# Performance work log

Hardware: AMD Instinct MI355X
Metric: run time of the kernel (lower is better)

The kernel has to match this reference:

```python
import jax, jax.numpy as jnp
import numpy as np


def _w2_1d(u, v):
    """Squared W2 distance between two 1D densities on grid positions arange(n)/n."""
    u = u / (jnp.sum(u) + 1e-10)
    v = v / (jnp.sum(v) + 1e-10)
    u_cdf = jnp.cumsum(u)                       # [n]
    v_cdf = jnp.cumsum(v)                       # [n]
    qs = jnp.sort(jnp.concatenate([u_cdf, v_cdf]))  # [2n]
    n = u.shape[0]
    pos = jnp.arange(n, dtype=u.dtype) / n      # support positions (n == m here)
    # quantile functions via searchsorted (side='left', same as torch default) + clamped gather
    u_q = pos[jnp.clip(jnp.searchsorted(u_cdf, qs), 0, n - 1)]
    v_q = pos[jnp.clip(jnp.searchsorted(v_cdf, qs), 0, n - 1)]
    delta = jnp.diff(qs, prepend=0.0)           # qs padded with leading zero, then diff
    return jnp.sum(delta * (u_q - v_q) ** 2)    # p = 2


def setup_inputs() -> dict:
    key = jax.random.key(0)
    k1, k2 = jax.random.split(key)
    B, S, T, R = 4, 8, 2048, 256
    x = jax.random.normal(k1, (B, S, T, R), dtype=jnp.float32)
    y = jax.random.normal(k2, (B, S, T, R), dtype=jnp.float32)
    return {"x": x, "y": y}


def reference(x, y):
    B, S, T, R = x.shape
    # transform_nonnegative, method='linear': shift by 1.1 * global min (if negative)
    mn = jnp.minimum(jnp.min(x), jnp.min(y))
    mn = jnp.where(mn < 0, mn, jnp.zeros((), x.dtype))
    x = x - 1.1 * mn
    y = y - 1.1 * mn
    # normalize along time axis (dim=2), sum-to-1
    x = x / jnp.sum(x, axis=2, keepdims=True)
    y = y / jnp.sum(y, axis=2, keepdims=True)
    # flatten (B, S, R) problems; each 1D distribution lives along the time axis
    xr = jnp.transpose(x, (0, 1, 3, 2)).reshape(-1, T)  # [B*S*R, T]
    yr = jnp.transpose(y, (0, 1, 3, 2)).reshape(-1, T)
    w2 = jax.vmap(_w2_1d)(xr, yr).reshape(B, S, R)
    return jnp.sum(w2, axis=(1, 2))  # loss per batch element, shape [B]
```

## Files before the change

### kernel.cpp

```cpp
#include <hip/hip_runtime.h>

#define T_N 2048
#define R_N 256
#define SLICES 32
#define NELEM (SLICES * T_N * R_N)
#define INFV 3.0e38f
#define MIN_BLOCKS 2048
#define MIN_THREADS (MIN_BLOCKS * 256)
#define LSTR 2056

#define XS(e) ((e) ^ (((e) >> 5) & 31))

__global__ __launch_bounds__(256) void kmin(const float* __restrict__ x,
                                            const float* __restrict__ y,
                                            float* __restrict__ partial,
                                            float* __restrict__ out) {
    if (blockIdx.x == 0 && threadIdx.x < 4) out[threadIdx.x] = 0.0f;
    const int g0 = blockIdx.x * 256 + threadIdx.x;
    const float4* __restrict__ x4 = (const float4*)x;
    const float4* __restrict__ y4 = (const float4*)y;
    float m0 = INFV, m1 = INFV;
    #pragma unroll
    for (int half = 0; half < 2; ++half) {
        float4 va[4], vb[4];
        #pragma unroll
        for (int it = 0; it < 4; ++it) {
            const int idx = g0 + (half * 4 + it) * MIN_THREADS;
            va[it] = x4[idx];
            vb[it] = y4[idx];
        }
        #pragma unroll
        for (int it = 0; it < 4; ++it) {
            m0 = fminf(m0, fminf(fminf(va[it].x, va[it].y), fminf(va[it].z, va[it].w)));
            m1 = fminf(m1, fminf(fminf(vb[it].x, vb[it].y), fminf(vb[it].z, vb[it].w)));
        }
    }
    float m = fminf(m0, m1);
    #pragma unroll
    for (int off = 32; off; off >>= 1) m = fminf(m, __shfl_down(m, off));
    __shared__ float sm[4];
    if ((threadIdx.x & 63) == 0) sm[threadIdx.x >> 6] = m;
    __syncthreads();
    if (threadIdx.x == 0)
        partial[blockIdx.x] = fminf(fminf(sm[0], sm[1]), fminf(sm[2], sm[3]));
}

__global__ __launch_bounds__(1024, 8) void kmain(const float* __restrict__ x,
                                                 const float* __restrict__ y,
                                                 const float* __restrict__ partial,
                                                 float* __restrict__ out) {
    __shared__ float L[8 * LSTR];
    __shared__ float red16[16];
    __shared__ float psum[4][2][4];
    __shared__ float pacc[4][4];

    const int tid = threadIdx.x;
    const int w = tid >> 6;
    const int lane = tid & 63;

    {
        float m = fminf(partial[tid], partial[tid + 1024]);
        #pragma unroll
        for (int off = 32; off; off >>= 1) m = fminf(m, __shfl_down(m, off));
        if (lane == 0) red16[w] = m;
    }
    __syncthreads();
    float mn = red16[0];
    #pragma unroll
    for (int k = 1; k < 16; ++k) mn = fminf(mn, red16[k]);
    const float sh = 1.1f * fminf(mn, 0.0f);

    const int blk = blockIdx.x;
    const int xcd = blk & 7;
    const int k2 = blk >> 3;
    const int sub = k2 & 3;
    const int rest = k2 >> 2;
    const int rt = (((rest & 1) << 3) + xcd) * 4 + sub;
    const int bs = rest >> 1;
    const size_t base = (size_t)bs * (T_N * R_N) + (size_t)(rt * 4);

    if (tid < 64) L[(tid >> 3) * LSTR + T_N + (tid & 7)] = INFV;

    #pragma unroll
    for (int it = 0; it < 2; ++it) {
        const int t = tid + 1024 * it;
        const int ts = XS(t);
        const float4 a = *(const float4*)(x + base + (size_t)t * R_N);
        const float4 b = *(const float4*)(y + base + (size_t)t * R_N);
        L[0 * LSTR + ts] = a.x - sh;  L[2 * LSTR + ts] = a.y - sh;
        L[4 * LSTR + ts] = a.z - sh;  L[6 * LSTR + ts] = a.w - sh;
        L[1 * LSTR + ts] = b.x - sh;  L[3 * LSTR + ts] = b.y - sh;
        L[5 * LSTR + ts] = b.z - sh;  L[7 * LSTR + ts] = b.w - sh;
    }
    __syncthreads();

    const int p  = w >> 2;
    const int wl = w & 3;
    const int pl = (wl << 6) | lane;
    float* __restrict__ cu = &L[(2 * p) * LSTR];
    float* __restrict__ cv = &L[(2 * p + 1) * LSTR];

    {
        int off8[8];
        #pragma unroll
        for (int k = 0; k < 8; ++k) off8[k] = XS(8 * pl + k);
        float uu[8], vv8[8];
        float su = 0.f, sv = 0.f;
        #pragma unroll
        for (int k = 0; k < 8; ++k) { uu[k] = cu[off8[k]]; su += uu[k]; }
        #pragma unroll
        for (int k = 0; k < 8; ++k) { vv8[k] = cv[off8[k]]; sv += vv8[k]; }
        float iu = su, iv = sv;
        #pragma unroll
        for (int off = 1; off < 64; off <<= 1) {
            const float a = __shfl_up(iu, off);
            const float b = __shfl_up(iv, off);
            if (lane >= off) { iu += a; iv += b; }
        }
        if (lane == 63) { psum[p][0][wl] = iu; psum[p][1][wl] = iv; }
        __syncthreads();
        float prefU = 0.f, totU = 0.f, prefV = 0.f, totV = 0.f;
        #pragma unroll
        for (int k = 0; k < 4; ++k) {
            const float a = psum[p][0][k], b = psum[p][1][k];
            totU += a; totV += b;
            if (k < wl) { prefU += a; prefV += b; }
        }
        const float invU = 1.0f / totU, invV = 1.0f / totV;
        float ru = prefU + (iu - su);
        float rv = prefV + (iv - sv);
        #pragma unroll
        for (int k = 0; k < 8; ++k) { ru += uu[k];  cu[off8[k]] = ru * invU; }
        #pragma unroll
        for (int k = 0; k < 8; ++k) { rv += vv8[k]; cv[off8[k]] = rv * invV; }
    }
    __syncthreads();

    const int d = pl << 4;
    int i = 0, j = 0;
    if (d > 0) {
        int lo = (d > T_N) ? (d - T_N) : 0;
        int hi = (d < T_N) ? d : T_N;
        while (lo < hi) {
            const int mid = (lo + hi) >> 1;
            if (cu[XS(mid)] <= cv[XS(d - mid - 1)]) lo = mid + 1; else hi = mid;
        }
        i = lo; j = d - lo;
    }
    float qprev = 0.0f;
    if (d > 0) {
        const float pa_ = (i > 0) ? cu[XS(i - 1)] : -INFV;
        const float pb_ = (j > 0) ? cv[XS(j - 1)] : -INFV;
        qprev = fmaxf(pa_, pb_);
    }

    float uv = cu[XS(i)];
    float vv = cv[XS(j)];
    float acc = 0.0f;
    #pragma unroll
    for (int s = 0; s < 16; ++s) {
        const bool take = (uv <= vv);
        const float q = fminf(uv, vv);
        const float dd = (float)(min(i, T_N - 1) - min(j, T_N - 1));
        acc += (q - qprev) * dd * dd;
        qprev = q;
        i += take ? 1 : 0;
        j += take ? 0 : 1;
        if (s < 15) {
            const int ni = take ? i : j;
            const float* bp = take ? cu : cv;
            const float r = bp[XS(ni)];
            uv = take ? r : uv;
            vv = take ? vv : r;
        }
    }

    #pragma unroll
    for (int off = 32; off; off >>= 1) acc += __shfl_down(acc, off);
    if (lane == 0) pacc[p][wl] = acc;
    __syncthreads();
    if (tid == 0) {
        float r = 0.f;
        #pragma unroll
        for (int pp = 0; pp < 4; ++pp)
            r += (pacc[pp][0] + pacc[pp][1]) + (pacc[pp][2] + pacc[pp][3]);
        atomicAdd(&out[bs >> 3], r * (1.0f / ((float)T_N * (float)T_N)));
    }
}

extern "C" void kernel_launch(void* const* d_in, const int* in_sizes, int n_in,
                              void* d_out, int out_size, void* d_ws, size_t ws_size,
                              hipStream_t stream) {
    const float* x = (const float*)d_in[0];
    const float* y = (const float*)d_in[1];
    float* out = (float*)d_out;
    float* partial = (float*)d_ws;

    kmin<<<MIN_BLOCKS, 256, 0, stream>>>(x, y, partial, out);
    kmain<<<SLICES * 64, 1024, 0, stream>>>(x, y, partial, out);
}
```

Measured before the change: 210.7 us.

## Overlap global loads with min reduction, use DPP and float2 LDS accesses

Issues the four float4 global loads for each thread's two adjacent time rows before the global-min reduction, so load latency overlaps the partial-min reduce and the first barrier. The shuffle-based min reduction is replaced with DPP row operations. The LDS swizzle is changed to keep element pairs adjacent, which allows float2 LDS stores during staging and float2 loads and stores in the cumulative-sum phase. Each thread now handles consecutive rows rather than strided ones, which changes the global coalescing pattern. This also risks bank conflicts under the new swizzle.

```diff
diff --git a/kernel.cpp b/kernel.cpp
--- a/kernel.cpp
+++ b/kernel.cpp
@@ -9,7 +9,11 @@
 #define MIN_THREADS (MIN_BLOCKS * 256)
 #define LSTR 2056
 
-#define XS(e) ((e) ^ (((e) >> 5) & 31))
+#define XS(e) ((e) ^ (((e) >> 4) & 30))
+
+#define DPPMIN(x, ctrl, rmask)                                                 \
+    fminf((x), __int_as_float(__builtin_amdgcn_update_dpp(                     \
+        0x7f800000, __float_as_int(x), (ctrl), (rmask), 0xf, false)))
 
 __global__ __launch_bounds__(256) void kmin(const float* __restrict__ x,
                                             const float* __restrict__ y,
@@ -49,7 +53,7 @@
                                                  const float* __restrict__ y,
                                                  const float* __restrict__ partial,
                                                  float* __restrict__ out) {
-    __shared__ float L[8 * LSTR];
+    __shared__ __align__(16) float L[8 * LSTR];
     __shared__ float red16[16];
     __shared__ float psum[4][2][4];
     __shared__ float pacc[4][4];
@@ -57,18 +61,6 @@
     const int tid = threadIdx.x;
     const int w = tid >> 6;
     const int lane = tid & 63;
-
-    {
-        float m = fminf(partial[tid], partial[tid + 1024]);
-        #pragma unroll
-        for (int off = 32; off; off >>= 1) m = fminf(m, __shfl_down(m, off));
-        if (lane == 0) red16[w] = m;
-    }
-    __syncthreads();
-    float mn = red16[0];
-    #pragma unroll
-    for (int k = 1; k < 16; ++k) mn = fminf(mn, red16[k]);
-    const float sh = 1.1f * fminf(mn, 0.0f);
 
     const int blk = blockIdx.x;
     const int xcd = blk & 7;
@@ -79,18 +71,39 @@
     const int bs = rest >> 1;
     const size_t base = (size_t)bs * (T_N * R_N) + (size_t)(rt * 4);
 
+    const int r0 = tid << 1;
+    const float4 a0 = *(const float4*)(x + base + (size_t)r0 * R_N);
+    const float4 a1 = *(const float4*)(x + base + (size_t)(r0 + 1) * R_N);
+    const float4 b0 = *(const float4*)(y + base + (size_t)r0 * R_N);
+    const float4 b1 = *(const float4*)(y + base + (size_t)(r0 + 1) * R_N);
+
+    {
+        float m = fminf(partial[tid], partial[tid + 1024]);
+        m = DPPMIN(m, 0x111, 0xf);
+        m = DPPMIN(m, 0x112, 0xf);
+        m = DPPMIN(m, 0x114, 0xf);
+        m = DPPMIN(m, 0x118, 0xf);
+        m = DPPMIN(m, 0x142, 0xa);
+        m = DPPMIN(m, 0x143, 0xc);
+        if (lane == 63) red16[w] = m;
+    }
     if (tid < 64) L[(tid >> 3) * LSTR + T_N + (tid & 7)] = INFV;
-
-    #pragma unroll
-    for (int it = 0; it < 2; ++it) {
-        const int t = tid + 1024 * it;
-        const int ts = XS(t);
-        const float4 a = *(const float4*)(x + base + (size_t)t * R_N);
-        const float4 b = *(const float4*)(y + base + (size_t)t * R_N);
-        L[0 * LSTR + ts] = a.x - sh;  L[2 * LSTR + ts] = a.y - sh;
-        L[4 * LSTR + ts] = a.z - sh;  L[6 * LSTR + ts] = a.w - sh;
-        L[1 * LSTR + ts] = b.x - sh;  L[3 * LSTR + ts] = b.y - sh;
-        L[5 * LSTR + ts] = b.z - sh;  L[7 * LSTR + ts] = b.w - sh;
+    __syncthreads();
+    float mn = red16[0];
+    #pragma unroll
+    for (int k = 1; k < 16; ++k) mn = fminf(mn, red16[k]);
+    const float sh = 1.1f * fminf(mn, 0.0f);
+
+    {
+        const int ws_ = XS(r0);
+        *(float2*)&L[0 * LSTR + ws_] = make_float2(a0.x - sh, a1.x - sh);
+        *(float2*)&L[2 * LSTR + ws_] = make_float2(a0.y - sh, a1.y - sh);
+        *(float2*)&L[4 * LSTR + ws_] = make_float2(a0.z - sh, a1.z - sh);
+        *(float2*)&L[6 * LSTR + ws_] = make_float2(a0.w - sh, a1.w - sh);
+        *(float2*)&L[1 * LSTR + ws_] = make_float2(b0.x - sh, b1.x - sh);
+        *(float2*)&L[3 * LSTR + ws_] = make_float2(b0.y - sh, b1.y - sh);
+        *(float2*)&L[5 * LSTR + ws_] = make_float2(b0.z - sh, b1.z - sh);
+        *(float2*)&L[7 * LSTR + ws_] = make_float2(b0.w - sh, b1.w - sh);
     }
     __syncthreads();
 
@@ -101,15 +114,25 @@
     float* __restrict__ cv = &L[(2 * p + 1) * LSTR];
 
     {
-        int off8[8];
-        #pragma unroll
-        for (int k = 0; k < 8; ++k) off8[k] = XS(8 * pl + k);
+        int offp[4];
+        #pragma unroll
+        for (int c = 0; c < 4; ++c) offp[c] = XS(8 * pl + 2 * c);
         float uu[8], vv8[8];
         float su = 0.f, sv = 0.f;
         #pragma unroll
-        for (int k = 0; k < 8; ++k) { uu[k] = cu[off8[k]]; su += uu[k]; }
-        #pragma unroll
-        for (int k = 0; k < 8; ++k) { vv8[k] = cv[off8[k]]; sv += vv8[k]; }
+        for (int c = 0; c < 4; ++c) {
+            const float2 t2 = *(const float2*)&cu[offp[c]];
+            uu[2 * c] = t2.x; uu[2 * c + 1] = t2.y;
+        }
+        #pragma unroll
+        for (int k = 0; k < 8; ++k) su += uu[k];
+        #pragma unroll
+        for (int c = 0; c < 4; ++c) {
+            const float2 t2 = *(const float2*)&cv[offp[c]];
+            vv8[2 * c] = t2.x; vv8[2 * c + 1] = t2.y;
+        }
+        #pragma unroll
+        for (int k = 0; k < 8; ++k) sv += vv8[k];
         float iu = su, iv = sv;
         #pragma unroll
         for (int off = 1; off < 64; off <<= 1) {
@@ -130,9 +153,19 @@
         float ru = prefU + (iu - su);
         float rv = prefV + (iv - sv);
         #pragma unroll
-        for (int k = 0; k < 8; ++k) { ru += uu[k];  cu[off8[k]] = ru * invU; }
-        #pragma unroll
-        for (int k = 0; k < 8; ++k) { rv += vv8[k]; cv[off8[k]] = rv * invV; }
+        for (int c = 0; c < 4; ++c) {
+            const float ra = ru + uu[2 * c];
+            const float rb = ra + uu[2 * c + 1];
+            ru = rb;
+            *(float2*)&cu[offp[c]] = make_float2(ra * invU, rb * invU);
+        }
+        #pragma unroll
+        for (int c = 0; c < 4; ++c) {
+            const float ra = rv + vv8[2 * c];
+            const float rb = ra + vv8[2 * c + 1];
+            rv = rb;
+            *(float2*)&cv[offp[c]] = make_float2(ra * invV, rb * invV);
+        }
     }
     __syncthreads();
 
```

New measurement: 198.4 us. -5.8%, faster.

## Issue global loads before min reduction and vectorize LDS transposed writes

Applied to the files above, without the earlier changes.

Global loads of the tile are issued before the global-min reduction so their latency overlaps the partial-min reduce, which now uses DPP row ops instead of shuffles. Each thread loads four consecutive time rows of one tensor and writes float4 chunks into LDS with a new XOR swizzle (XQ). The scan phase reads with float4 LDS loads under that swizzle. kmin is also restructured to issue all 16 loads up front. The cost is more registers held across the barrier and a more intricate swizzle that has to stay consistent with the later XS-based reads.

```diff
diff --git a/kernel.cpp b/kernel.cpp
--- a/kernel.cpp
+++ b/kernel.cpp
@@ -10,6 +10,11 @@
 #define LSTR 2056
 
 #define XS(e) ((e) ^ (((e) >> 5) & 31))
+#define XQ(e) ((e) ^ (((e) >> 3) & 28))
+
+#define DPPMIN(x, ctrl, rmask)                                                 \
+    fminf((x), __int_as_float(__builtin_amdgcn_update_dpp(                     \
+        0x7f800000, __float_as_int(x), (ctrl), (rmask), 0xf, false)))
 
 __global__ __launch_bounds__(256) void kmin(const float* __restrict__ x,
                                             const float* __restrict__ y,
@@ -19,22 +24,18 @@
     const int g0 = blockIdx.x * 256 + threadIdx.x;
     const float4* __restrict__ x4 = (const float4*)x;
     const float4* __restrict__ y4 = (const float4*)y;
+    float4 va[8], vb[8];
+    #pragma unroll
+    for (int it = 0; it < 8; ++it) va[it] = x4[g0 + it * MIN_THREADS];
+    #pragma unroll
+    for (int it = 0; it < 8; ++it) vb[it] = y4[g0 + it * MIN_THREADS];
     float m0 = INFV, m1 = INFV;
     #pragma unroll
-    for (int half = 0; half < 2; ++half) {
-        float4 va[4], vb[4];
-        #pragma unroll
-        for (int it = 0; it < 4; ++it) {
-            const int idx = g0 + (half * 4 + it) * MIN_THREADS;
-            va[it] = x4[idx];
-            vb[it] = y4[idx];
-        }
-        #pragma unroll
-        for (int it = 0; it < 4; ++it) {
-            m0 = fminf(m0, fminf(fminf(va[it].x, va[it].y), fminf(va[it].z, va[it].w)));
-            m1 = fminf(m1, fminf(fminf(vb[it].x, vb[it].y), fminf(vb[it].z, vb[it].w)));
-        }
-    }
+    for (int it = 0; it < 8; ++it)
+        m0 = fminf(m0, fminf(fminf(va[it].x, va[it].y), fminf(va[it].z, va[it].w)));
+    #pragma unroll
+    for (int it = 0; it < 8; ++it)
+        m1 = fminf(m1, fminf(fminf(vb[it].x, vb[it].y), fminf(vb[it].z, vb[it].w)));
     float m = fminf(m0, m1);
     #pragma unroll
     for (int off = 32; off; off >>= 1) m = fminf(m, __shfl_down(m, off));
@@ -49,26 +50,14 @@
                                                  const float* __restrict__ y,
                                                  const float* __restrict__ partial,
                                                  float* __restrict__ out) {
-    __shared__ float L[8 * LSTR];
-    __shared__ float red16[16];
-    __shared__ float psum[4][2][4];
-    __shared__ float pacc[4][4];
+    __shared__ __align__(16) float L[8 * LSTR];
+    __shared__ __align__(16) float red16[16];
+    __shared__ __align__(16) float psum[4][2][4];
+    __shared__ __align__(16) float pacc[4][4];
 
     const int tid = threadIdx.x;
     const int w = tid >> 6;
     const int lane = tid & 63;
-
-    {
-        float m = fminf(partial[tid], partial[tid + 1024]);
-        #pragma unroll
-        for (int off = 32; off; off >>= 1) m = fminf(m, __shfl_down(m, off));
-        if (lane == 0) red16[w] = m;
-    }
-    __syncthreads();
-    float mn = red16[0];
-    #pragma unroll
-    for (int k = 1; k < 16; ++k) mn = fminf(mn, red16[k]);
-    const float sh = 1.1f * fminf(mn, 0.0f);
 
     const int blk = blockIdx.x;
     const int xcd = blk & 7;
@@ -79,18 +68,48 @@
     const int bs = rest >> 1;
     const size_t base = (size_t)bs * (T_N * R_N) + (size_t)(rt * 4);
 
+    const int st = tid & 511;
+    const int r0 = st << 2;
+    const int lb = tid >> 9;
+    const float* __restrict__ src = (lb == 0) ? x : y;
+    const float4 g0v = *(const float4*)(src + base + (size_t)(r0 + 0) * R_N);
+    const float4 g1v = *(const float4*)(src + base + (size_t)(r0 + 1) * R_N);
+    const float4 g2v = *(const float4*)(src + base + (size_t)(r0 + 2) * R_N);
+    const float4 g3v = *(const float4*)(src + base + (size_t)(r0 + 3) * R_N);
+
+    {
+        float m = fminf(partial[tid], partial[tid + 1024]);
+        m = DPPMIN(m, 0x111, 0xf);
+        m = DPPMIN(m, 0x112, 0xf);
+        m = DPPMIN(m, 0x114, 0xf);
+        m = DPPMIN(m, 0x118, 0xf);
+        m = DPPMIN(m, 0x142, 0xa);
+        m = DPPMIN(m, 0x143, 0xc);
+        if (lane == 63) red16[w] = m;
+    }
     if (tid < 64) L[(tid >> 3) * LSTR + T_N + (tid & 7)] = INFV;
-
-    #pragma unroll
-    for (int it = 0; it < 2; ++it) {
-        const int t = tid + 1024 * it;
-        const int ts = XS(t);
-        const float4 a = *(const float4*)(x + base + (size_t)t * R_N);
-        const float4 b = *(const float4*)(y + base + (size_t)t * R_N);
-        L[0 * LSTR + ts] = a.x - sh;  L[2 * LSTR + ts] = a.y - sh;
-        L[4 * LSTR + ts] = a.z - sh;  L[6 * LSTR + ts] = a.w - sh;
-        L[1 * LSTR + ts] = b.x - sh;  L[3 * LSTR + ts] = b.y - sh;
-        L[5 * LSTR + ts] = b.z - sh;  L[7 * LSTR + ts] = b.w - sh;
+    __syncthreads();
+    const float4 q0 = *(const float4*)&red16[0];
+    const float4 q1 = *(const float4*)&red16[4];
+    const float4 q2 = *(const float4*)&red16[8];
+    const float4 q3 = *(const float4*)&red16[12];
+    const float mn =
+        fminf(fminf(fminf(fminf(q0.x, q0.y), fminf(q0.z, q0.w)),
+                    fminf(fminf(q1.x, q1.y), fminf(q1.z, q1.w))),
+              fminf(fminf(fminf(q2.x, q2.y), fminf(q2.z, q2.w)),
+                    fminf(fminf(q3.x, q3.y), fminf(q3.z, q3.w))));
+    const float sh = 1.1f * fminf(mn, 0.0f);
+
+    {
+        const int wq = r0 ^ ((r0 >> 3) & 28);
+        *(float4*)&L[(0 + lb) * LSTR + wq] =
+            make_float4(g0v.x - sh, g1v.x - sh, g2v.x - sh, g3v.x - sh);
+        *(float4*)&L[(2 + lb) * LSTR + wq] =
+            make_float4(g0v.y - sh, g1v.y - sh, g2v.y - sh, g3v.y - sh);
+        *(float4*)&L[(4 + lb) * LSTR + wq] =
+            make_float4(g0v.z - sh, g1v.z - sh, g2v.z - sh, g3v.z - sh);
+        *(float4*)&L[(6 + lb) * LSTR + wq] =
+            make_float4(g0v.w - sh, g1v.w - sh, g2v.w - sh, g3v.w - sh);
     }
     __syncthreads();
 
@@ -101,15 +120,25 @@
     float* __restrict__ cv = &L[(2 * p + 1) * LSTR];
 
     {
-        int off8[8];
-        #pragma unroll
-        for (int k = 0; k < 8; ++k) off8[k] = XS(8 * pl + k);
+        const int rq = (8 * pl) ^ (pl & 28);
         float uu[8], vv8[8];
+        {
+            const float4 t0 = *(const float4*)&cu[rq];
+            const float4 t1 = *(const float4*)&cu[rq ^ 4];
+            uu[0] = t0.x; uu[1] = t0.y; uu[2] = t0.z; uu[3] = t0.w;
+            uu[4] = t1.x; uu[5] = t1.y; uu[6] = t1.z; uu[7] = t1.w;
+        }
         float su = 0.f, sv = 0.f;
         #pragma unroll
-        for (int k = 0; k < 8; ++k) { uu[k] = cu[off8[k]]; su += uu[k]; }
-        #pragma unroll
-        for (int k = 0; k < 8; ++k) { vv8[k] = cv[off8[k]]; sv += vv8[k]; }
+        for (int k = 0; k < 8; ++k) su += uu[k];
+        {
+            const float4 t0 = *(const float4*)&cv[rq];
+            const float4 t1 = *(const float4*)&cv[rq ^ 4];
+            vv8[0] = t0.x; vv8[1] = t0.y; vv8[2] = t0.z; vv8[3] = t0.w;
+            vv8[4] = t1.x; vv8[5] = t1.y; vv8[6] = t1.z; vv8[7] = t1.w;
+        }
+        #pragma unroll
+        for (int k = 0; k < 8; ++k) sv += vv8[k];
         float iu = su, iv = sv;
         #pragma unroll
         for (int off = 1; off < 64; off <<= 1) {
@@ -119,20 +148,24 @@
         }
         if (lane == 63) { psum[p][0][wl] = iu; psum[p][1][wl] = iv; }
         __syncthreads();
+        const float4 pu4 = *(const float4*)&psum[p][0][0];
+        const float4 pv4 = *(const float4*)&psum[p][1][0];
+        const float puA[4] = {pu4.x, pu4.y, pu4.z, pu4.w};
+        const float pvA[4] = {pv4.x, pv4.y, pv4.z, pv4.w};
         float prefU = 0.f, totU = 0.f, prefV = 0.f, totV = 0.f;
         #pragma unroll
         for (int k = 0; k < 4; ++k) {
-            const float a = psum[p][0][k], b = psum[p][1][k];
-            totU += a; totV += b;
-            if (k < wl) { prefU += a; prefV += b; }
+            totU += puA[k]; totV += pvA[k];
+            if (k < wl) { prefU += puA[k]; prefV += pvA[k]; }
         }
         const float invU = 1.0f / totU, invV = 1.0f / totV;
         float ru = prefU + (iu - su);
         float rv = prefV + (iv - sv);
-        #pragma unroll
-        for (int k = 0; k < 8; ++k) { ru += uu[k];  cu[off8[k]] = ru * invU; }
-        #pragma unroll
-        for (int k = 0; k < 8; ++k) { rv += vv8[k]; cv[off8[k]] = rv * invV; }
+        const int cm = (pl >> 2) & 31;
+        #pragma unroll
+        for (int k = 0; k < 8; ++k) { ru += uu[k];  cu[(8 * pl + k) ^ cm] = ru * invU; }
+        #pragma unroll
+        for (int k = 0; k < 8; ++k) { rv += vv8[k]; cv[(8 * pl + k) ^ cm] = rv * invV; }
     }
     __syncthreads();
 
@@ -182,8 +215,10 @@
     if (tid == 0) {
         float r = 0.f;
         #pragma unroll
-        for (int pp = 0; pp < 4; ++pp)
-            r += (pacc[pp][0] + pacc[pp][1]) + (pacc[pp][2] + pacc[pp][3]);
+        for (int pp = 0; pp < 4; ++pp) {
+            const float4 pa4 = *(const float4*)&pacc[pp][0];
+            r += (pa4.x + pa4.y) + (pa4.z + pa4.w);
+        }
         atomicAdd(&out[bs >> 3], r * (1.0f / ((float)T_N * (float)T_N)));
     }
 }
```

Result: faster. 206.2 us (-2.2%).
